# Performance work log

Hardware: AMD Instinct MI355X
Metric: run time of the kernel (lower is better)

The kernel has to match this reference:

```python
import jax, jax.numpy as jnp
import numpy as np


def setup_inputs() -> dict:
    key = jax.random.key(0)
    k1, k2 = jax.random.split(key)
    B, R1, R2, D = 16, 2048, 2048, 256
    matrix_1 = jax.random.normal(k1, (B, R1, D), dtype=jnp.float32)
    matrix_2 = jax.random.normal(k2, (B, R2, D), dtype=jnp.float32)
    return {"matrix_1": matrix_1, "matrix_2": matrix_2}


def reference(matrix_1, matrix_2):
    # Original keras layer tiles matrix_1 to [B, R1, R2, D] and matrix_2 to
    # [B, R1, R2, D], then applies the dot-product similarity (elementwise
    # multiply + sum over last dim). That is exactly a batched matmul:
    #   scores[b, i, j] = sum_d matrix_1[b, i, d] * matrix_2[b, j, d]
    return jnp.einsum('bid,bjd->bij', matrix_1, matrix_2)
```

## Files before the change

### kernel.cpp

```cpp
#include <hip/hip_runtime.h>
#include <hip/hip_bf16.h>
#include <stdint.h>


typedef _Float16 f16x8 __attribute__((ext_vector_type(8)));
typedef _Float16 f16x4 __attribute__((ext_vector_type(4)));
typedef _Float16 f16x2 __attribute__((ext_vector_type(2)));
typedef float f32x4 __attribute__((ext_vector_type(4)));

#define NB 16
#define DM 2048
#define DN 2048
#define DK 256
#define BM 128
#define BN 128
#define BK 32
#define BKP 36
#define NT (DK / BK)
#define NWG (NB * (DM/BM) * (DN/BN))

__global__ __launch_bounds__(256, 2) void fused_gemm(const float* __restrict__ A,
                                                     const float* __restrict__ B,
                                                     float* __restrict__ C) {
    __shared__ _Float16 As[2][BM * BKP];
    __shared__ _Float16 Bs[2][BN * BKP];

    const int t = threadIdx.x;

    const int bid = blockIdx.x;
    const int swz = (bid & 7) * (NWG / 8) + (bid >> 3);
    const int b    = swz >> 8;
    const int rem  = swz & 255;
    const int brow = (rem >> 4) << 7;
    const int bcol = (rem & 15) << 7;

    const float* At = A + (size_t)b * DM * DK + (size_t)brow * DK;
    const float* Bt = B + (size_t)b * DN * DK + (size_t)bcol * DK;

    const int w    = t >> 6;
    const int l    = t & 63;
    const int wr   = (w >> 1) * 64;
    const int wc   = (w & 1) * 64;
    const int lrow = l & 15;
    const int lko  = (l >> 4) * 8;

    f32x4 acc[4][4] = {};

    auto issue = [&](int kt, float4 (&va)[4], float4 (&vb)[4]) {
#pragma unroll
        for (int i = 0; i < 4; ++i) {
            const int c = t + i * 256;
            const int r = c >> 3, q = c & 7;
            va[i] = *reinterpret_cast<const float4*>(At + (size_t)r * DK + kt * BK + q * 4);
            vb[i] = *reinterpret_cast<const float4*>(Bt + (size_t)r * DK + kt * BK + q * 4);
        }
    };
    auto wlds = [&](int buf, const float4 (&va)[4], const float4 (&vb)[4]) {
#pragma unroll
        for (int i = 0; i < 4; ++i) {
            const int c = t + i * 256;
            const int r = c >> 3, q = c & 7;
            f16x2 alo = __builtin_bit_cast(f16x2, __builtin_amdgcn_cvt_pkrtz(va[i].x, va[i].y));
            f16x2 ahi = __builtin_bit_cast(f16x2, __builtin_amdgcn_cvt_pkrtz(va[i].z, va[i].w));
            f16x2 blo = __builtin_bit_cast(f16x2, __builtin_amdgcn_cvt_pkrtz(vb[i].x, vb[i].y));
            f16x2 bhi = __builtin_bit_cast(f16x2, __builtin_amdgcn_cvt_pkrtz(vb[i].z, vb[i].w));
            f16x4 ha = { alo[0], alo[1], ahi[0], ahi[1] };
            f16x4 hb = { blo[0], blo[1], bhi[0], bhi[1] };
            *reinterpret_cast<f16x4*>(&As[buf][r * BKP + q * 4]) = ha;
            *reinterpret_cast<f16x4*>(&Bs[buf][r * BKP + q * 4]) = hb;
        }
    };
    auto compute = [&](int buf) {
        f16x8 af[4], bfr[4];
#pragma unroll
        for (int m = 0; m < 4; ++m)
            af[m] = *reinterpret_cast<const f16x8*>(&As[buf][(wr + m * 16 + lrow) * BKP + lko]);
#pragma unroll
        for (int n = 0; n < 4; ++n)
            bfr[n] = *reinterpret_cast<const f16x8*>(&Bs[buf][(wc + n * 16 + lrow) * BKP + lko]);
#pragma unroll
        for (int m = 0; m < 4; ++m)
#pragma unroll
            for (int n = 0; n < 4; ++n)
                acc[m][n] = __builtin_amdgcn_mfma_f32_16x16x32_f16(af[m], bfr[n], acc[m][n], 0, 0, 0);
    };

    float4 vaX[4], vbX[4], vaY[4], vbY[4];

    issue(0, vaX, vbX);
    issue(1, vaY, vbY);
    wlds(0, vaX, vbX);
    __syncthreads();

#pragma unroll
    for (int k2 = 0; k2 < NT; k2 += 2) {
        if (k2 + 2 < NT) issue(k2 + 2, vaX, vbX);
        compute(0);
        wlds(1, vaY, vbY);
        __syncthreads();

        if (k2 + 3 < NT) issue(k2 + 3, vaY, vbY);
        compute(1);
        if (k2 + 2 < NT) {
            wlds(0, vaX, vbX);
        }
        __syncthreads();
    }

    float* Cb = C + (size_t)b * DM * DN;
    const int crow = brow + wr + (l >> 4) * 4;
    const int ccol = bcol + wc + lrow;
#pragma unroll
    for (int m = 0; m < 4; ++m)
#pragma unroll
        for (int j = 0; j < 4; ++j) {
            float* rowp = Cb + (size_t)(crow + m * 16 + j) * DN + ccol;
#pragma unroll
            for (int n = 0; n < 4; ++n)
                __builtin_nontemporal_store(acc[m][n][j], rowp + n * 16);
        }
}

extern "C" void kernel_launch(void* const* d_in, const int* in_sizes, int n_in,
                              void* d_out, int out_size, void* d_ws, size_t ws_size,
                              hipStream_t stream) {
    const float* m1 = (const float*)d_in[0];
    const float* m2 = (const float*)d_in[1];
    float* out = (float*)d_out;
    (void)d_ws; (void)ws_size;

    fused_gemm<<<NWG, 256, 0, stream>>>(m1, m2, out);
}
```

Measured before the change: 75.77 us.

## Make GEMM workgroups persistent over four column tiles with continuous prefetch

Each workgroup now computes four consecutive 128x128 output tiles along N, 1024 workgroups instead of 4096, in one flattened K-step loop. Global loads for the next tile are issued while the current tile finishes, and each tile's results are stored inside the loop. This is meant to hide the prologue/epilogue load latency and launch tail of short per-tile work. The trade-off is fewer workgroups (1024 on 256 CUs at 2 per CU) and a non-unrolled loop carrying extra control logic.

```diff
diff --git a/kernel.cpp b/kernel.cpp
--- a/kernel.cpp
+++ b/kernel.cpp
@@ -16,8 +16,10 @@
 #define BN 128
 #define BK 32
 #define BKP 36
-#define NT (DK / BK)
-#define NWG (NB * (DM/BM) * (DN/BN))
+#define NT 8
+#define NTILES 4
+#define TSTEPS (NT * NTILES)
+#define NWG 1024
 
 __global__ __launch_bounds__(256, 2) void fused_gemm(const float* __restrict__ A,
                                                      const float* __restrict__ B,
@@ -29,13 +31,13 @@
 
     const int bid = blockIdx.x;
     const int swz = (bid & 7) * (NWG / 8) + (bid >> 3);
-    const int b    = swz >> 8;
-    const int rem  = swz & 255;
-    const int brow = (rem >> 4) << 7;
-    const int bcol = (rem & 15) << 7;
+    const int b    = swz >> 6;
+    const int rem  = swz & 63;
+    const int brow = (rem >> 2) << 7;
+    const int grp  = rem & 3;
 
-    const float* At = A + (size_t)b * DM * DK + (size_t)brow * DK;
-    const float* Bt = B + (size_t)b * DN * DK + (size_t)bcol * DK;
+    const float* At  = A + (size_t)b * DM * DK + (size_t)brow * DK;
+    const float* Bt0 = B + (size_t)b * DN * DK + (size_t)(grp << 9) * DK;
 
     const int w    = t >> 6;
     const int l    = t & 63;
@@ -46,13 +48,15 @@
 
     f32x4 acc[4][4] = {};
 
-    auto issue = [&](int kt, float4 (&va)[4], float4 (&vb)[4]) {
+    auto issue = [&](int s, float4 (&va)[4], float4 (&vb)[4]) {
+        const float* Ap = At + (size_t)(s & 7) * BK;
+        const float* Bp = Bt0 + (size_t)(s >> 3) * BM * DK + (size_t)(s & 7) * BK;
 #pragma unroll
         for (int i = 0; i < 4; ++i) {
             const int c = t + i * 256;
             const int r = c >> 3, q = c & 7;
-            va[i] = *reinterpret_cast<const float4*>(At + (size_t)r * DK + kt * BK + q * 4);
-            vb[i] = *reinterpret_cast<const float4*>(Bt + (size_t)r * DK + kt * BK + q * 4);
+            va[i] = *reinterpret_cast<const float4*>(Ap + (size_t)r * DK + q * 4);
+            vb[i] = *reinterpret_cast<const float4*>(Bp + (size_t)r * DK + q * 4);
         }
     };
     auto wlds = [&](int buf, const float4 (&va)[4], const float4 (&vb)[4]) {
@@ -85,6 +89,22 @@
                 acc[m][n] = __builtin_amdgcn_mfma_f32_16x16x32_f16(af[m], bfr[n], acc[m][n], 0, 0, 0);
     };
 
+    float* Cb = C + (size_t)b * DM * DN;
+    const int crow0 = brow + wr + (l >> 4) * 4;
+    const int ccol0 = (grp << 9) + wc + lrow;
+    auto store_tile = [&](int tile) {
+        const int ccol = ccol0 + tile * BN;
+#pragma unroll
+        for (int m = 0; m < 4; ++m)
+#pragma unroll
+            for (int j = 0; j < 4; ++j) {
+                float* rowp = Cb + (size_t)(crow0 + m * 16 + j) * DN + ccol;
+#pragma unroll
+                for (int n = 0; n < 4; ++n)
+                    __builtin_nontemporal_store(acc[m][n][j], rowp + n * 16);
+            }
+    };
+
     float4 vaX[4], vbX[4], vaY[4], vbY[4];
 
     issue(0, vaX, vbX);
@@ -92,33 +112,32 @@
     wlds(0, vaX, vbX);
     __syncthreads();
 
+#pragma unroll 1
+    for (int s2 = 0; s2 < TSTEPS; s2 += 2) {
+        if (s2 + 2 < TSTEPS) issue(s2 + 2, vaX, vbX);
+
+        if (s2 > 0 && (s2 & 7) == 0) {
 #pragma unroll
-    for (int k2 = 0; k2 < NT; k2 += 2) {
-        if (k2 + 2 < NT) issue(k2 + 2, vaX, vbX);
+            for (int m = 0; m < 4; ++m)
+#pragma unroll
+                for (int n = 0; n < 4; ++n) acc[m][n] = f32x4{0.f, 0.f, 0.f, 0.f};
+        }
+
         compute(0);
         wlds(1, vaY, vbY);
         __syncthreads();
 
-        if (k2 + 3 < NT) issue(k2 + 3, vaY, vbY);
+        if (s2 + 3 < TSTEPS) issue(s2 + 3, vaY, vbY);
         compute(1);
-        if (k2 + 2 < NT) {
-            wlds(0, vaX, vbX);
+
+        if ((s2 & 7) == 6) {
+            store_tile((s2 + 1) >> 3);
+            __builtin_amdgcn_sched_barrier(0);
         }
+
+        if (s2 + 2 < TSTEPS) wlds(0, vaX, vbX);
         __syncthreads();
     }
-
-    float* Cb = C + (size_t)b * DM * DN;
-    const int crow = brow + wr + (l >> 4) * 4;
-    const int ccol = bcol + wc + lrow;
-#pragma unroll
-    for (int m = 0; m < 4; ++m)
-#pragma unroll
-        for (int j = 0; j < 4; ++j) {
-            float* rowp = Cb + (size_t)(crow + m * 16 + j) * DN + ccol;
-#pragma unroll
-            for (int n = 0; n < 4; ++n)
-                __builtin_nontemporal_store(acc[m][n][j], rowp + n * 16);
-        }
 }
 
 extern "C" void kernel_launch(void* const* d_in, const int* in_sizes, int n_in,
```

Measured after the change: 85.93 us. 1.13x slower.
